# Kernel tuning notes

Hardware: AMD Instinct MI355X
Metric: run time of the kernel (lower is better)

Reference implementation:

```python
import jax, jax.numpy as jnp
import numpy as np

NUM_ITERS = 20  # fixed in the original forward: transcribe(dna, iterations=20)


def transcribe(dna_seed, dna_a, dna_b):
    """Fractal DNA decompression: 20 elementwise contractive-map iterations
    over the full weight tensor, starting from the DNA seed."""
    def step(w, ab):
        a, b = ab
        w = a * w + b * jnp.sin(w)
        return w, None
    w, _ = jax.lax.scan(step, dna_seed, (dna_a, dna_b))
    return w  # [out_features, in_features]


def setup_inputs() -> dict:
    key = jax.random.key(0)
    k1, k2, k3, k4, k5 = jax.random.split(key, 5)
    TOKENS, IN_F, OUT_F = 2048, 4096, 4096
    return {
        "x": jax.random.normal(k1, (TOKENS, IN_F), dtype=jnp.float32),
        "dna_seed": jax.random.normal(k2, (OUT_F, IN_F), dtype=jnp.float32),
        "dna_a": jax.random.uniform(k3, (NUM_ITERS,), dtype=jnp.float32),
        "dna_b": jax.random.uniform(k4, (NUM_ITERS,), dtype=jnp.float32),
        "bias": jax.random.normal(k5, (OUT_F,), dtype=jnp.float32),
    }


def reference(x, dna_seed, dna_a, dna_b, bias):
    weight = transcribe(dna_seed, dna_a, dna_b)          # [out, in]
    # F.linear(x, weight, bias) == x @ weight.T + bias
    return jnp.einsum('ti,oi->to', x, weight) + bias     # [tokens, out]
```

## Files before the change

kernel.cpp:

```cpp
#include <hip/hip_runtime.h>
#include <hip/hip_bf16.h>

typedef __attribute__((ext_vector_type(8))) short short8;
typedef __attribute__((ext_vector_type(4))) float floatx4;

#define TOKENS 2048
#define IN_F   4096
#define OUT_F  4096
#define NITER  20

#define INV_2PI 0.15915494309189535f
#define TWO_PI  6.283185307179586f

__device__ __forceinline__ unsigned short f2bf(float f) {
    unsigned int u = __builtin_bit_cast(unsigned int, f);
    u += 0x7fffu + ((u >> 16) & 1u);
    return (unsigned short)(u >> 16);
}

__device__ __forceinline__ void step4(float4& v, float a, float bc) {
    v.x = __builtin_fmaf(bc, __builtin_amdgcn_sinf(v.x), a * v.x);
    v.y = __builtin_fmaf(bc, __builtin_amdgcn_sinf(v.y), a * v.y);
    v.z = __builtin_fmaf(bc, __builtin_amdgcn_sinf(v.z), a * v.z);
    v.w = __builtin_fmaf(bc, __builtin_amdgcn_sinf(v.w), a * v.w);
}

template <int ITERS>
__global__ __launch_bounds__(256) void transcribe_kernel(
    const float4* __restrict__ in,
    const float* __restrict__ da, const float* __restrict__ db,
    short8* __restrict__ out, int n8)
{
    int i = blockIdx.x * 256 + threadIdx.x;
    if (i >= n8) return;
    float4 u = in[2 * i];
    float4 v = in[2 * i + 1];
    float fin = 1.0f;
    if (ITERS > 0) {
        u.x *= INV_2PI; u.y *= INV_2PI; u.z *= INV_2PI; u.w *= INV_2PI;
        v.x *= INV_2PI; v.y *= INV_2PI; v.z *= INV_2PI; v.w *= INV_2PI;
#pragma unroll
        for (int t = 0; t < ITERS; t++) {
            float a = da[t], bc = db[t] * INV_2PI;
            step4(u, a, bc);
            step4(v, a, bc);
        }
        fin = TWO_PI;
    }
    short8 o;
    o[0] = (short)f2bf(u.x * fin); o[1] = (short)f2bf(u.y * fin);
    o[2] = (short)f2bf(u.z * fin); o[3] = (short)f2bf(u.w * fin);
    o[4] = (short)f2bf(v.x * fin); o[5] = (short)f2bf(v.y * fin);
    o[6] = (short)f2bf(v.z * fin); o[7] = (short)f2bf(v.w * fin);
    out[i] = o;
}

__device__ __forceinline__ void g2l16(const ushort* g, ushort* l) {
    __builtin_amdgcn_global_load_lds(
        (const __attribute__((address_space(1))) unsigned int*)g,
        (__attribute__((address_space(3))) unsigned int*)l, 16, 0, 0);
}

__global__ __launch_bounds__(256) void gemm_bt_kernel(
    const ushort* __restrict__ A,
    const ushort* __restrict__ B,
    const float* __restrict__ bias,
    float* __restrict__ C,
    int M, int N, int K)
{
    __shared__ ushort As[64 * 32];
    __shared__ ushort Bs[128 * 32];

    const int tid  = threadIdx.x;
    const int lane = tid & 63;
    const int wid  = tid >> 6;
    const int bn   = blockIdx.x;
    const int bm   = blockIdx.y;
    const int wm   = (wid >> 1) << 5;
    const int wn   = (wid & 1) << 6;
    const int fm   = lane & 15;
    const int fkd  = (((lane >> 4) ^ ((fm >> 1) & 3)) << 3);

    const int row0 = tid >> 2;
    const int psg  = tid & 3;
    const int gsg  = (psg ^ ((row0 >> 1) & 3)) << 3;
    const int lsg  = psg << 3;

    const ushort* gA = A + (size_t)(bm * 64) * K;
    const ushort* gB = B + (size_t)(bn * 128) * K;

    floatx4 acc[2][4];
#pragma unroll
    for (int i = 0; i < 2; i++)
#pragma unroll
        for (int j = 0; j < 4; j++)
            acc[i][j] = (floatx4){0.f, 0.f, 0.f, 0.f};

    for (int k0 = 0; k0 < K; k0 += 32) {
        g2l16(gA + (size_t)row0 * K + k0 + gsg,        As + row0 * 32 + lsg);
        g2l16(gB + (size_t)row0 * K + k0 + gsg,        Bs + row0 * 32 + lsg);
        g2l16(gB + (size_t)(row0 + 64) * K + k0 + gsg, Bs + (row0 + 64) * 32 + lsg);
        __syncthreads();

        short8 af[2], bfr[4];
#pragma unroll
        for (int i = 0; i < 2; i++)
            af[i] = *(const short8*)(As + (wm + i * 16 + fm) * 32 + fkd);
#pragma unroll
        for (int j = 0; j < 4; j++)
            bfr[j] = *(const short8*)(Bs + (wn + j * 16 + fm) * 32 + fkd);
#pragma unroll
        for (int i = 0; i < 2; i++)
#pragma unroll
            for (int j = 0; j < 4; j++)
                acc[i][j] = __builtin_amdgcn_mfma_f32_16x16x32_bf16(
                    af[i], bfr[j], acc[i][j], 0, 0, 0);
        __syncthreads();
    }

    const int cn = lane & 15;
    const int cm = (lane >> 4) << 2;
    float bv[4];
#pragma unroll
    for (int j = 0; j < 4; j++)
        bv[j] = bias[bn * 128 + wn + j * 16 + cn];
#pragma unroll
    for (int i = 0; i < 2; i++) {
#pragma unroll
        for (int r = 0; r < 4; r++) {
            int m = bm * 64 + wm + i * 16 + cm + r;
            float* crow = C + (size_t)m * N + bn * 128 + wn + cn;
#pragma unroll
            for (int j = 0; j < 4; j++)
                crow[j * 16] = acc[i][j][r] + bv[j];
        }
    }
}

extern "C" void kernel_launch(void* const* d_in, const int* in_sizes, int n_in,
                              void* d_out, int out_size, void* d_ws, size_t ws_size,
                              hipStream_t stream) {
    const float* x    = (const float*)d_in[0];
    const float* seed = (const float*)d_in[1];
    const float* da   = (const float*)d_in[2];
    const float* db   = (const float*)d_in[3];
    const float* bias = (const float*)d_in[4];
    float* out        = (float*)d_out;

    ushort* w_bf = (ushort*)d_ws;
    ushort* x_bf = w_bf + (size_t)OUT_F * IN_F;

    const int n8_w = OUT_F * IN_F / 8;
    const int n8_x = TOKENS * IN_F / 8;

    transcribe_kernel<NITER><<<n8_w / 256, 256, 0, stream>>>(
        (const float4*)seed, da, db, (short8*)w_bf, n8_w);
    transcribe_kernel<0><<<n8_x / 256, 256, 0, stream>>>(
        (const float4*)x, da, db, (short8*)x_bf, n8_x);

    dim3 grid(OUT_F / 128, TOKENS / 64);
    gemm_bt_kernel<<<grid, 256, 0, stream>>>(x_bf, w_bf, bias, out,
                                             TOKENS, OUT_F, IN_F);
}
```

Baseline: 242.3 us.

## Enlarge GEMM tile to 128x128x64 with LDS double buffering and fuse conversion kernels

Each GEMM block now computes a 128x128 tile instead of 64x128, with BK raised to 64. It double-buffers LDS so global-to-LDS loads for the next K slice overlap the MFMA work on the current one, and uses a new XOR swizzle for bank-conflict avoidance. The weight transcription and x conversion are merged into one launch to save a kernel launch. The larger tile raises arithmetic intensity and cuts sync count per K, at the cost of more LDS (64KB) and more accumulator registers, which may lower occupancy.

```diff
diff --git a/kernel.cpp b/kernel.cpp
--- a/kernel.cpp
+++ b/kernel.cpp
@@ -1,5 +1,4 @@
 #include <hip/hip_runtime.h>
-#include <hip/hip_bf16.h>
 
 typedef __attribute__((ext_vector_type(8))) short short8;
 typedef __attribute__((ext_vector_type(4))) float floatx4;
@@ -8,6 +7,7 @@
 #define IN_F   4096
 #define OUT_F  4096
 #define NITER  20
+#define BK     64
 
 #define INV_2PI 0.15915494309189535f
 #define TWO_PI  6.283185307179586f
@@ -25,34 +25,43 @@
     v.w = __builtin_fmaf(bc, __builtin_amdgcn_sinf(v.w), a * v.w);
 }
 
-template <int ITERS>
-__global__ __launch_bounds__(256) void transcribe_kernel(
-    const float4* __restrict__ in,
+#define WBLOCKS (OUT_F * IN_F / 8 / 256)
+#define XBLOCKS (TOKENS * IN_F / 8 / 256)
+
+__global__ __launch_bounds__(256) void transcribe_fused_kernel(
+    const float4* __restrict__ seed, const float4* __restrict__ xin,
     const float* __restrict__ da, const float* __restrict__ db,
-    short8* __restrict__ out, int n8)
+    short8* __restrict__ w_out, short8* __restrict__ x_out)
 {
-    int i = blockIdx.x * 256 + threadIdx.x;
-    if (i >= n8) return;
-    float4 u = in[2 * i];
-    float4 v = in[2 * i + 1];
-    float fin = 1.0f;
-    if (ITERS > 0) {
+    const int b = blockIdx.x;
+    short8 o;
+    if (b < WBLOCKS) {
+        int i = b * 256 + threadIdx.x;
+        float4 u = seed[2 * i];
+        float4 v = seed[2 * i + 1];
         u.x *= INV_2PI; u.y *= INV_2PI; u.z *= INV_2PI; u.w *= INV_2PI;
         v.x *= INV_2PI; v.y *= INV_2PI; v.z *= INV_2PI; v.w *= INV_2PI;
 #pragma unroll
-        for (int t = 0; t < ITERS; t++) {
+        for (int t = 0; t < NITER; t++) {
             float a = da[t], bc = db[t] * INV_2PI;
             step4(u, a, bc);
             step4(v, a, bc);
         }
-        fin = TWO_PI;
+        o[0] = (short)f2bf(u.x * TWO_PI); o[1] = (short)f2bf(u.y * TWO_PI);
+        o[2] = (short)f2bf(u.z * TWO_PI); o[3] = (short)f2bf(u.w * TWO_PI);
+        o[4] = (short)f2bf(v.x * TWO_PI); o[5] = (short)f2bf(v.y * TWO_PI);
+        o[6] = (short)f2bf(v.z * TWO_PI); o[7] = (short)f2bf(v.w * TWO_PI);
+        w_out[i] = o;
+    } else {
+        int i = (b - WBLOCKS) * 256 + threadIdx.x;
+        float4 u = xin[2 * i];
+        float4 v = xin[2 * i + 1];
+        o[0] = (short)f2bf(u.x); o[1] = (short)f2bf(u.y);
+        o[2] = (short)f2bf(u.z); o[3] = (short)f2bf(u.w);
+        o[4] = (short)f2bf(v.x); o[5] = (short)f2bf(v.y);
+        o[6] = (short)f2bf(v.z); o[7] = (short)f2bf(v.w);
+        x_out[i] = o;
     }
-    short8 o;
-    o[0] = (short)f2bf(u.x * fin); o[1] = (short)f2bf(u.y * fin);
-    o[2] = (short)f2bf(u.z * fin); o[3] = (short)f2bf(u.w * fin);
-    o[4] = (short)f2bf(v.x * fin); o[5] = (short)f2bf(v.y * fin);
-    o[6] = (short)f2bf(v.z * fin); o[7] = (short)f2bf(v.w * fin);
-    out[i] = o;
 }
 
 __device__ __forceinline__ void g2l16(const ushort* g, ushort* l) {
@@ -61,62 +70,87 @@
         (__attribute__((address_space(3))) unsigned int*)l, 16, 0, 0);
 }
 
-__global__ __launch_bounds__(256) void gemm_bt_kernel(
+__global__ __launch_bounds__(256, 2) void gemm_bt_kernel(
     const ushort* __restrict__ A,
     const ushort* __restrict__ B,
     const float* __restrict__ bias,
-    float* __restrict__ C,
-    int M, int N, int K)
+    float* __restrict__ C)
 {
-    __shared__ ushort As[64 * 32];
-    __shared__ ushort Bs[128 * 32];
+    __shared__ ushort As[2][128 * BK];
+    __shared__ ushort Bs[2][128 * BK];
 
     const int tid  = threadIdx.x;
     const int lane = tid & 63;
     const int wid  = tid >> 6;
     const int bn   = blockIdx.x;
     const int bm   = blockIdx.y;
-    const int wm   = (wid >> 1) << 5;
+    const int wm   = (wid >> 1) << 6;
     const int wn   = (wid & 1) << 6;
     const int fm   = lane & 15;
-    const int fkd  = (((lane >> 4) ^ ((fm >> 1) & 3)) << 3);
+    const int q    = lane >> 4;
 
-    const int row0 = tid >> 2;
-    const int psg  = tid & 3;
-    const int gsg  = (psg ^ ((row0 >> 1) & 3)) << 3;
-    const int lsg  = psg << 3;
+    const int gcol = (((lane & 7) ^ (lane >> 3)) << 3);
 
-    const ushort* gA = A + (size_t)(bm * 64) * K;
-    const ushort* gB = B + (size_t)(bn * 128) * K;
+    const ushort* gA = A + (size_t)(bm * 128) * IN_F;
+    const ushort* gB = B + (size_t)(bn * 128) * IN_F;
 
-    floatx4 acc[2][4];
+    floatx4 acc[4][4];
 #pragma unroll
-    for (int i = 0; i < 2; i++)
+    for (int i = 0; i < 4; i++)
 #pragma unroll
         for (int j = 0; j < 4; j++)
             acc[i][j] = (floatx4){0.f, 0.f, 0.f, 0.f};
 
-    for (int k0 = 0; k0 < K; k0 += 32) {
-        g2l16(gA + (size_t)row0 * K + k0 + gsg,        As + row0 * 32 + lsg);
-        g2l16(gB + (size_t)row0 * K + k0 + gsg,        Bs + row0 * 32 + lsg);
-        g2l16(gB + (size_t)(row0 + 64) * K + k0 + gsg, Bs + (row0 + 64) * 32 + lsg);
+#define STAGE(k0v, bufi)                                                      \
+    {                                                                         \
+        _Pragma("unroll")                                                     \
+        for (int u = 0; u < 4; u++) {                                         \
+            const int cb = ((u << 2) | wid) << 6;             \
+            const int r  = (cb >> 3) + (lane >> 3);           \
+            g2l16(gA + (size_t)r * IN_F + (k0v) + gcol,                       \
+                  &As[bufi][cb * 8 + lane * 8]);                              \
+            g2l16(gB + (size_t)r * IN_F + (k0v) + gcol,                       \
+                  &Bs[bufi][cb * 8 + lane * 8]);                              \
+        }                                                                     \
+    }
+
+#define COMPUTE(bufi)                                                         \
+    {                                                                         \
+        _Pragma("unroll")                                                     \
+        for (int s = 0; s < 2; s++) {                                         \
+            short8 af[4], bf[4];                                              \
+            const int sa = (((q + 4 * s) & 7) ^ (fm & 7)) << 3;               \
+            _Pragma("unroll")                                                 \
+            for (int i = 0; i < 4; i++) {                                     \
+                af[i] = *(const short8*)&As[bufi][(wm + i * 16 + fm) * BK + sa]; \
+                bf[i] = *(const short8*)&Bs[bufi][(wn + i * 16 + fm) * BK + sa]; \
+            }                                                                 \
+            _Pragma("unroll")                                                 \
+            for (int i = 0; i < 4; i++)                                       \
+                _Pragma("unroll")                                             \
+                for (int j = 0; j < 4; j++)                                   \
+                    acc[i][j] = __builtin_amdgcn_mfma_f32_16x16x32_bf16(      \
+                        af[i], bf[j], acc[i][j], 0, 0, 0);                    \
+        }                                                                     \
+    }
+
+    STAGE(0, 0);
+    __syncthreads();
+    STAGE(BK, 1);
+    COMPUTE(0);
+    __syncthreads();
+    for (int k0 = 2 * BK; k0 < IN_F; k0 += 2 * BK) {
+        STAGE(k0, 0);
+        COMPUTE(1);
         __syncthreads();
-
-        short8 af[2], bfr[4];
-#pragma unroll
-        for (int i = 0; i < 2; i++)
-            af[i] = *(const short8*)(As + (wm + i * 16 + fm) * 32 + fkd);
-#pragma unroll
-        for (int j = 0; j < 4; j++)
-            bfr[j] = *(const short8*)(Bs + (wn + j * 16 + fm) * 32 + fkd);
-#pragma unroll
-        for (int i = 0; i < 2; i++)
-#pragma unroll
-            for (int j = 0; j < 4; j++)
-                acc[i][j] = __builtin_amdgcn_mfma_f32_16x16x32_bf16(
-                    af[i], bfr[j], acc[i][j], 0, 0, 0);
+        STAGE(k0 + BK, 1);
+        COMPUTE(0);
         __syncthreads();
     }
+    COMPUTE(1);
+
+#undef STAGE
+#undef COMPUTE
 
     const int cn = lane & 15;
     const int cm = (lane >> 4) << 2;
@@ -125,11 +159,11 @@
     for (int j = 0; j < 4; j++)
         bv[j] = bias[bn * 128 + wn + j * 16 + cn];
 #pragma unroll
-    for (int i = 0; i < 2; i++) {
+    for (int i = 0; i < 4; i++) {
 #pragma unroll
         for (int r = 0; r < 4; r++) {
-            int m = bm * 64 + wm + i * 16 + cm + r;
-            float* crow = C + (size_t)m * N + bn * 128 + wn + cn;
+            int m = bm * 128 + wm + i * 16 + cm + r;
+            float* crow = C + (size_t)m * OUT_F + bn * 128 + wn + cn;
 #pragma unroll
             for (int j = 0; j < 4; j++)
                 crow[j * 16] = acc[i][j][r] + bv[j];
@@ -150,15 +184,10 @@
     ushort* w_bf = (ushort*)d_ws;
     ushort* x_bf = w_bf + (size_t)OUT_F * IN_F;
 
-    const int n8_w = OUT_F * IN_F / 8;
-    const int n8_x = TOKENS * IN_F / 8;
+    transcribe_fused_kernel<<<WBLOCKS + XBLOCKS, 256, 0, stream>>>(
+        (const float4*)seed, (const float4*)x, da, db,
+        (short8*)w_bf, (short8*)x_bf);
 
-    transcribe_kernel<NITER><<<n8_w / 256, 256, 0, stream>>>(
-        (const float4*)seed, da, db, (short8*)w_bf, n8_w);
-    transcribe_kernel<0><<<n8_x / 256, 256, 0, stream>>>(
-        (const float4*)x, da, db, (short8*)x_bf, n8_x);
-
-    dim3 grid(OUT_F / 128, TOKENS / 64);
-    gemm_bt_kernel<<<grid, 256, 0, stream>>>(x_bf, w_bf, bias, out,
-                                             TOKENS, OUT_F, IN_F);
+    dim3 grid(OUT_F / 128, TOKENS / 128);
+    gemm_bt_kernel<<<grid, 256, 0, stream>>>(x_bf, w_bf, bias, out);
 }
```

Result: faster. 215.8 us, median of 2 (-10.9%).
